# Performance work log

Measured on AMD Instinct MI355X. Metric: run time of the kernel, lower is better.

Reference implementation:

```python
import jax, jax.numpy as jnp
import numpy as np

# Dims: lifted grid is N_X x N_Y, input signal has N_IN dims (= N_X*N_Y).
N_X, N_Y, N_IN = 32, 32, 1024
FILT = 33              # resolution-filter taps (odd, centered)
SIGMA0 = 0.1           # resolution_filter_initial_sigma (step 0 of decay schedule)
EPS = 1e-7


def _resolution_filter(sigma):
    # Gaussian taps on normalized coords in ~[-1, 1], normalized to sum 1.
    t = (jnp.arange(FILT, dtype=jnp.float32) - FILT // 2) * (2.0 / FILT)
    k = jnp.exp(-0.5 * jnp.square(t / sigma))
    return k / jnp.sum(k)


def _interpolate_lifting_map(lm_raw, filt):
    # Circular 1-D convolution of the generator parametrization with the
    # Gaussian resolution filter along the input-signal axis.
    P = N_X * N_Y
    pad = FILT // 2
    v = lm_raw.reshape(P, 1, N_IN)
    v = jnp.concatenate([v[..., -pad:], v, v[..., :pad]], axis=-1)  # wrap pad
    k = filt.reshape(1, 1, FILT)
    out = jax.lax.conv_general_dilated(
        v, k, window_strides=(1,), padding='VALID',
        dimension_numbers=('NCH', 'OIH', 'NCH'))
    return out.reshape(N_X, N_Y, N_IN)


def setup_inputs() -> dict:
    key = jax.random.key(0)
    k1, k2 = jax.random.split(key)
    x = jax.random.normal(k1, (16384, N_IN), dtype=jnp.float32)
    lm_raw = jax.random.normal(k2, (N_X, N_Y, N_IN), dtype=jnp.float32) / np.float32(np.sqrt(N_IN))
    return {"x": x, "lm_raw": lm_raw}


def reference(x, lm_raw):
    # _demean_and_normalize_input: per-sample demean + std-normalize.
    mu = jnp.mean(x, axis=-1, keepdims=True)
    sd = jnp.std(x, axis=-1, keepdims=True)
    xn = (x - mu) / (sd + EPS)
    # _sample_resolution_filter + _interpolate_lifting_map
    filt = _resolution_filter(jnp.asarray(SIGMA0, dtype=jnp.float32))
    lm = _interpolate_lifting_map(lm_raw, filt)  # [n_x, n_y, n_in]
    # _lift: y[b, i, j] = sum_n lm[i, j, n] * x[b, n]
    y = jnp.einsum('xyn,bn->bxy', lm, xn)
    return y
```

## Files before the change

### kernel.cpp

```cpp
#include <hip/hip_runtime.h>
#include <hip/hip_bf16.h>

#define N_IN   1024
#define N_P    1024
#define FILT   33
#define PAD    16

typedef __attribute__((ext_vector_type(8))) __bf16 bf16x8;
typedef __attribute__((ext_vector_type(4))) float  f32x4;

#define GLB(p) ((const __attribute__((address_space(1))) unsigned int*)(p))
#define LDSP(p) ((__attribute__((address_space(3))) unsigned int*)(p))

__device__ __forceinline__ unsigned short f2bf(float f) {
    union { __hip_bfloat16 h; unsigned short u; } cv;
    cv.h = __float2bfloat16(f);
    return cv.u;
}

__global__ __launch_bounds__(256)
void normalize_kernel(const float* __restrict__ x, __hip_bfloat16* __restrict__ xn)
{
    const int lane = threadIdx.x & 63;
    const int row  = blockIdx.x * 4 + (threadIdx.x >> 6);

    const float4* xr = reinterpret_cast<const float4*>(x + (size_t)row * N_IN);
    float4 v[4];
    float s = 0.f, s2 = 0.f;
#pragma unroll
    for (int i = 0; i < 4; i++) {
        v[i] = xr[i * 64 + lane];
        s  += v[i].x + v[i].y + v[i].z + v[i].w;
        s2 += v[i].x * v[i].x + v[i].y * v[i].y + v[i].z * v[i].z + v[i].w * v[i].w;
    }
#pragma unroll
    for (int off = 32; off > 0; off >>= 1) {
        s  += __shfl_xor(s,  off, 64);
        s2 += __shfl_xor(s2, off, 64);
    }
    const float mu  = s * (1.0f / N_IN);
    const float var = fmaxf(s2 * (1.0f / N_IN) - mu * mu, 0.0f);
    const float inv = 1.0f / (sqrtf(var) + 1e-7f);

    ushort4* outv = reinterpret_cast<ushort4*>(xn + (size_t)row * N_IN);
#pragma unroll
    for (int i = 0; i < 4; i++) {
        ushort4 o;
        o.x = f2bf((v[i].x - mu) * inv);
        o.y = f2bf((v[i].y - mu) * inv);
        o.z = f2bf((v[i].z - mu) * inv);
        o.w = f2bf((v[i].w - mu) * inv);
        outv[i * 64 + lane] = o;
    }
}

__global__ __launch_bounds__(256)
void conv_kernel(const float* __restrict__ lm_raw, __hip_bfloat16* __restrict__ lm)
{
    __shared__ float row[N_IN];
    __shared__ float fw[FILT];
    const int tid = threadIdx.x;
    const int p   = blockIdx.x;

    if (tid < FILT) {
        float t = (tid - PAD) * (2.0f / FILT);
        float u = t * 10.0f;
        fw[tid] = expf(-0.5f * u * u);
    }
    reinterpret_cast<float4*>(row)[tid] =
        reinterpret_cast<const float4*>(lm_raw + (size_t)p * N_IN)[tid];
    __syncthreads();

    float fsum = 0.f;
#pragma unroll
    for (int f = 0; f < FILT; f++) fsum += fw[f];
    const float inv = 1.0f / fsum;

    const int n0 = tid * 4;
    float o[4] = {0.f, 0.f, 0.f, 0.f};
#pragma unroll
    for (int f = 0; f < FILT; f++) {
        const float w = fw[f];
#pragma unroll
        for (int j = 0; j < 4; j++)
            o[j] += w * row[(n0 + j + f - PAD) & (N_IN - 1)];
    }
    ushort4 ov;
    ov.x = f2bf(o[0] * inv);
    ov.y = f2bf(o[1] * inv);
    ov.z = f2bf(o[2] * inv);
    ov.w = f2bf(o[3] * inv);
    reinterpret_cast<ushort4*>(lm + (size_t)p * N_IN)[tid] = ov;
}

__global__ __launch_bounds__(512, 2)
void gemm_bt2(const __hip_bfloat16* __restrict__ A,
              const __hip_bfloat16* __restrict__ B,
              float* __restrict__ C,
              int M, int N, int K)
{
    constexpr int BK = 32;
    __shared__ char smem[4][32768];

    const int tid = threadIdx.x;
    const int l   = tid & 63;
    const int w   = tid >> 6;
    const int wr  = w >> 2;
    const int wc  = w & 3;

    const int o    = blockIdx.x;
    const int lin  = (o & 7) * (gridDim.x >> 3) + (o >> 3);
    const int tn   = lin & 3;
    const int tm   = lin >> 2;
    const size_t bm = (size_t)tm * 256;
    const size_t bn = (size_t)tn * 256;

    const int srow = w * 16 + (l >> 2);
    const int scol = 16 * ((l & 3) ^ ((l >> 3) & 3));
    const char* gA = (const char*)(A + (bm + srow) * (size_t)K) + scol;
    const char* gB = (const char*)(B + (bn + srow) * (size_t)K) + scol;
    const size_t rowstep = (size_t)128 * K * 2;

#define STAGE(t, b) do {                                                        \
    const char* a0_ = gA + (size_t)(t) * (BK * 2);                              \
    const char* b0_ = gB + (size_t)(t) * (BK * 2);                              \
    char* La_ = &smem[(b)][0]     + w * 1024;                                   \
    char* Lb_ = &smem[(b)][16384] + w * 1024;                                   \
    __builtin_amdgcn_global_load_lds(GLB(a0_),           LDSP(La_),        16, 0, 0); \
    __builtin_amdgcn_global_load_lds(GLB(a0_ + rowstep), LDSP(La_ + 8192), 16, 0, 0); \
    __builtin_amdgcn_global_load_lds(GLB(b0_),           LDSP(Lb_),        16, 0, 0); \
    __builtin_amdgcn_global_load_lds(GLB(b0_ + rowstep), LDSP(Lb_ + 8192), 16, 0, 0); \
} while (0)

    const int lr = l & 15;
    const int kb = l >> 4;
    const int rslot = 16 * (kb ^ ((lr >> 1) & 3));

    f32x4 acc[8][4] = {};

    const int NT = K / BK;

    STAGE(0, 0);
    STAGE(1, 1);
    STAGE(2, 2);

    for (int t = 0; t < NT; ++t) {
        asm volatile("s_waitcnt lgkmcnt(0)" ::: "memory");
        if (t < NT - 2)       asm volatile("s_waitcnt vmcnt(8)" ::: "memory");
        else if (t == NT - 2) asm volatile("s_waitcnt vmcnt(4)" ::: "memory");
        else                  asm volatile("s_waitcnt vmcnt(0)" ::: "memory");
        __builtin_amdgcn_s_barrier();
        asm volatile("" ::: "memory");

        if (t + 3 < NT) STAGE(t + 3, (t + 3) & 3);

        const char* Ab = &smem[t & 3][0];
        const char* Bb = &smem[t & 3][16384];

        bf16x8 bfr[4], afr[8];
#pragma unroll
        for (int n = 0; n < 4; n++)
            bfr[n] = *(const bf16x8*)(Bb + (wc * 64 + n * 16 + lr) * 64 + rslot);
#pragma unroll
        for (int m = 0; m < 8; m++)
            afr[m] = *(const bf16x8*)(Ab + (wr * 128 + m * 16 + lr) * 64 + rslot);

#pragma unroll
        for (int m = 0; m < 8; m++)
#pragma unroll
            for (int n = 0; n < 4; n++)
                acc[m][n] = __builtin_amdgcn_mfma_f32_16x16x32_bf16(afr[m], bfr[n], acc[m][n], 0, 0, 0);
    }
#undef STAGE

    const int crow = (l >> 4) * 4;
    const int ccol = l & 15;
#pragma unroll
    for (int m = 0; m < 8; m++)
#pragma unroll
        for (int n = 0; n < 4; n++) {
#pragma unroll
            for (int r = 0; r < 4; r++) {
                const size_t row = bm + wr * 128 + m * 16 + crow + r;
                const size_t col = bn + wc * 64 + n * 16 + ccol;
                C[row * N + col] = acc[m][n][r];
            }
        }
}

extern "C" void kernel_launch(void* const* d_in, const int* in_sizes, int n_in,
                              void* d_out, int out_size, void* d_ws, size_t ws_size,
                              hipStream_t stream) {
    const float* x      = (const float*)d_in[0];
    const float* lm_raw = (const float*)d_in[1];
    float* out = (float*)d_out;

    const int M = in_sizes[0] / N_IN;

    __hip_bfloat16* xn = (__hip_bfloat16*)d_ws;
    __hip_bfloat16* lm = (__hip_bfloat16*)((char*)d_ws + (size_t)M * N_IN * 2);

    normalize_kernel<<<M / 4, 256, 0, stream>>>(x, xn);
    conv_kernel<<<N_P, 256, 0, stream>>>(lm_raw, lm);

    const int nblk = (M / 256) * (N_P / 256);
    gemm_bt2<<<nblk, dim3(512), 0, stream>>>(xn, lm, out, M, N_P, N_IN);
}
```

Before: 65.58 us.

## Shrink GEMM tile to 256x128 with 3-stage LDS ring and higher occupancy

Changes the GEMM block tile from 256x256 to 256x128, rearranges the 8 waves as a 4x2 grid with 64x64 sub-tiles each, and cuts the LDS ring from 4 to 3 stages (prefetch distance 2). Launch bounds are raised to 4 blocks per CU and MFMA issue is wrapped in s_setprio. The aim is to double the block count and raise occupancy so latency is hidden by concurrent blocks, at the cost of more B-tile reloads per output element and a shallower prefetch pipeline.

New measurement: 65.77 us. About the same (+0.3%).

```diff
diff --git a/kernel.cpp b/kernel.cpp
--- a/kernel.cpp
+++ b/kernel.cpp
@@ -93,27 +93,27 @@
     reinterpret_cast<ushort4*>(lm + (size_t)p * N_IN)[tid] = ov;
 }
 
-__global__ __launch_bounds__(512, 2)
-void gemm_bt2(const __hip_bfloat16* __restrict__ A,
+__global__ __launch_bounds__(512, 4)
+void gemm_bt3(const __hip_bfloat16* __restrict__ A,
               const __hip_bfloat16* __restrict__ B,
               float* __restrict__ C,
               int M, int N, int K)
 {
     constexpr int BK = 32;
-    __shared__ char smem[4][32768];
+    __shared__ char smem[3][24576];
 
     const int tid = threadIdx.x;
     const int l   = tid & 63;
     const int w   = tid >> 6;
-    const int wr  = w >> 2;
-    const int wc  = w & 3;
+    const int wm  = w >> 1;
+    const int wn  = w & 1;
 
     const int o    = blockIdx.x;
     const int lin  = (o & 7) * (gridDim.x >> 3) + (o >> 3);
-    const int tn   = lin & 3;
-    const int tm   = lin >> 2;
+    const int tn   = lin & 7;
+    const int tm   = lin >> 3;
     const size_t bm = (size_t)tm * 256;
-    const size_t bn = (size_t)tn * 256;
+    const size_t bn = (size_t)tn * 128;
 
     const int srow = w * 16 + (l >> 2);
     const int scol = 16 * ((l & 3) ^ ((l >> 3) & 3));
@@ -129,60 +129,66 @@
     __builtin_amdgcn_global_load_lds(GLB(a0_),           LDSP(La_),        16, 0, 0); \
     __builtin_amdgcn_global_load_lds(GLB(a0_ + rowstep), LDSP(La_ + 8192), 16, 0, 0); \
     __builtin_amdgcn_global_load_lds(GLB(b0_),           LDSP(Lb_),        16, 0, 0); \
-    __builtin_amdgcn_global_load_lds(GLB(b0_ + rowstep), LDSP(Lb_ + 8192), 16, 0, 0); \
 } while (0)
 
     const int lr = l & 15;
     const int kb = l >> 4;
     const int rslot = 16 * (kb ^ ((lr >> 1) & 3));
-
-    f32x4 acc[8][4] = {};
+    const int abase = (wm * 64 + lr) * 64 + rslot;
+    const int bbase = 16384 + (wn * 64 + lr) * 64 + rslot;
+
+    f32x4 acc[4][4] = {};
 
     const int NT = K / BK;
 
     STAGE(0, 0);
     STAGE(1, 1);
-    STAGE(2, 2);
-
+
+    int buf = 0;
     for (int t = 0; t < NT; ++t) {
         asm volatile("s_waitcnt lgkmcnt(0)" ::: "memory");
-        if (t < NT - 2)       asm volatile("s_waitcnt vmcnt(8)" ::: "memory");
-        else if (t == NT - 2) asm volatile("s_waitcnt vmcnt(4)" ::: "memory");
-        else                  asm volatile("s_waitcnt vmcnt(0)" ::: "memory");
+        if (t < NT - 1) asm volatile("s_waitcnt vmcnt(3)" ::: "memory");
+        else            asm volatile("s_waitcnt vmcnt(0)" ::: "memory");
         __builtin_amdgcn_s_barrier();
         asm volatile("" ::: "memory");
 
-        if (t + 3 < NT) STAGE(t + 3, (t + 3) & 3);
-
-        const char* Ab = &smem[t & 3][0];
-        const char* Bb = &smem[t & 3][16384];
-
-        bf16x8 bfr[4], afr[8];
-#pragma unroll
-        for (int n = 0; n < 4; n++)
-            bfr[n] = *(const bf16x8*)(Bb + (wc * 64 + n * 16 + lr) * 64 + rslot);
-#pragma unroll
-        for (int m = 0; m < 8; m++)
-            afr[m] = *(const bf16x8*)(Ab + (wr * 128 + m * 16 + lr) * 64 + rslot);
-
-#pragma unroll
-        for (int m = 0; m < 8; m++)
+        {
+            const int t2 = t + 2;
+            if (t2 < NT) {
+                int b2 = buf + 2; if (b2 >= 3) b2 -= 3;
+                STAGE(t2, b2);
+            }
+        }
+
+        const char* Sb = &smem[buf][0];
+        bf16x8 afr[4], bfr[4];
+#pragma unroll
+        for (int n = 0; n < 4; n++) bfr[n] = *(const bf16x8*)(Sb + bbase + n * 1024);
+#pragma unroll
+        for (int m = 0; m < 4; m++) afr[m] = *(const bf16x8*)(Sb + abase + m * 1024);
+
+        __builtin_amdgcn_s_setprio(1);
+#pragma unroll
+        for (int m = 0; m < 4; m++)
 #pragma unroll
             for (int n = 0; n < 4; n++)
                 acc[m][n] = __builtin_amdgcn_mfma_f32_16x16x32_bf16(afr[m], bfr[n], acc[m][n], 0, 0, 0);
+        __builtin_amdgcn_s_setprio(0);
+
+        if (++buf == 3) buf = 0;
     }
 #undef STAGE
 
     const int crow = (l >> 4) * 4;
     const int ccol = l & 15;
 #pragma unroll
-    for (int m = 0; m < 8; m++)
+    for (int m = 0; m < 4; m++)
 #pragma unroll
         for (int n = 0; n < 4; n++) {
 #pragma unroll
             for (int r = 0; r < 4; r++) {
-                const size_t row = bm + wr * 128 + m * 16 + crow + r;
-                const size_t col = bn + wc * 64 + n * 16 + ccol;
+                const size_t row = bm + wm * 64 + m * 16 + crow + r;
+                const size_t col = bn + wn * 64 + n * 16 + ccol;
                 C[row * N + col] = acc[m][n][r];
             }
         }
@@ -203,6 +209,6 @@
     normalize_kernel<<<M / 4, 256, 0, stream>>>(x, xn);
     conv_kernel<<<N_P, 256, 0, stream>>>(lm_raw, lm);
 
-    const int nblk = (M / 256) * (N_P / 256);
-    gemm_bt2<<<nblk, dim3(512), 0, stream>>>(xn, lm, out, M, N_P, N_IN);
-}
+    const int nblk = (M / 256) * (N_P / 128);
+    gemm_bt3<<<nblk, dim3(512), 0, stream>>>(xn, lm, out, M, N_P, N_IN);
+}
```

## Make GEMM waves load their own LDS tiles and raise MFMA priority

Applied to the files above, without the earlier changes.

The GEMM staging changes so that each wave issues global-to-LDS loads only for the A rows and B rows it later reads. This removes the need for a block-wide lgkmcnt drain before the barrier. Prefetch depth drops from three tiles ahead to two, and each wave now waits only on its own vmcnt. The MFMA block is wrapped in s_setprio to favour compute issue. The cost is redundant loading: waves sharing rows or columns load and write the same data, which roughly triples per-block global-to-LDS traffic.

Result: slower. 75.61 us (+15.3%).

```diff
diff --git a/kernel.cpp b/kernel.cpp
--- a/kernel.cpp
+++ b/kernel.cpp
@@ -94,19 +94,18 @@
 }
 
 __global__ __launch_bounds__(512, 2)
-void gemm_bt2(const __hip_bfloat16* __restrict__ A,
-              const __hip_bfloat16* __restrict__ B,
-              float* __restrict__ C,
-              int M, int N, int K)
+void gemm_async(const __hip_bfloat16* __restrict__ A,
+                const __hip_bfloat16* __restrict__ B,
+                float* __restrict__ C,
+                int M, int N, int K)
 {
-    constexpr int BK = 32;
     __shared__ char smem[4][32768];
 
     const int tid = threadIdx.x;
     const int l   = tid & 63;
     const int w   = tid >> 6;
-    const int wr  = w >> 2;
-    const int wc  = w & 3;
+    const int wm  = w >> 2;
+    const int wn  = w & 3;
 
     const int o    = blockIdx.x;
     const int lin  = (o & 7) * (gridDim.x >> 3) + (o >> 3);
@@ -115,63 +114,67 @@
     const size_t bm = (size_t)tm * 256;
     const size_t bn = (size_t)tn * 256;
 
-    const int srow = w * 16 + (l >> 2);
+    const int sgrp = l >> 2;
     const int scol = 16 * ((l & 3) ^ ((l >> 3) & 3));
-    const char* gA = (const char*)(A + (bm + srow) * (size_t)K) + scol;
-    const char* gB = (const char*)(B + (bn + srow) * (size_t)K) + scol;
-    const size_t rowstep = (size_t)128 * K * 2;
-
-#define STAGE(t, b) do {                                                        \
-    const char* a0_ = gA + (size_t)(t) * (BK * 2);                              \
-    const char* b0_ = gB + (size_t)(t) * (BK * 2);                              \
-    char* La_ = &smem[(b)][0]     + w * 1024;                                   \
-    char* Lb_ = &smem[(b)][16384] + w * 1024;                                   \
-    __builtin_amdgcn_global_load_lds(GLB(a0_),           LDSP(La_),        16, 0, 0); \
-    __builtin_amdgcn_global_load_lds(GLB(a0_ + rowstep), LDSP(La_ + 8192), 16, 0, 0); \
-    __builtin_amdgcn_global_load_lds(GLB(b0_),           LDSP(Lb_),        16, 0, 0); \
-    __builtin_amdgcn_global_load_lds(GLB(b0_ + rowstep), LDSP(Lb_ + 8192), 16, 0, 0); \
+    const char* gAw = (const char*)(A + (bm + wm * 128 + sgrp) * (size_t)K) + scol;
+    const char* gBw = (const char*)(B + (bn + wn * 64  + sgrp) * (size_t)K) + scol;
+    const size_t chunkstep = (size_t)16 * K * 2;
+
+#define STAGE_W(t, b) do {                                                      \
+    const char* a_ = gAw + (size_t)(t) * 64;                                    \
+    const char* b_ = gBw + (size_t)(t) * 64;                                    \
+    char* L_ = &smem[(b)][0];                                                   \
+    _Pragma("unroll")                                                           \
+    for (int c_ = 0; c_ < 8; c_++)                                              \
+        __builtin_amdgcn_global_load_lds(GLB(a_ + c_ * chunkstep),              \
+            LDSP(L_ + wm * 8192 + c_ * 1024), 16, 0, 0);                        \
+    _Pragma("unroll")                                                           \
+    for (int c_ = 0; c_ < 4; c_++)                                              \
+        __builtin_amdgcn_global_load_lds(GLB(b_ + c_ * chunkstep),              \
+            LDSP(L_ + 16384 + wn * 4096 + c_ * 1024), 16, 0, 0);                \
 } while (0)
 
     const int lr = l & 15;
     const int kb = l >> 4;
     const int rslot = 16 * (kb ^ ((lr >> 1) & 3));
+    const int abase = (wm * 128 + lr) * 64 + rslot;
+    const int bbase = 16384 + (wn * 64 + lr) * 64 + rslot;
 
     f32x4 acc[8][4] = {};
-
-    const int NT = K / BK;
-
-    STAGE(0, 0);
-    STAGE(1, 1);
-    STAGE(2, 2);
+    const int NT = K / 32;
+
+    STAGE_W(0, 0);
+    STAGE_W(1, 1);
 
     for (int t = 0; t < NT; ++t) {
-        asm volatile("s_waitcnt lgkmcnt(0)" ::: "memory");
-        if (t < NT - 2)       asm volatile("s_waitcnt vmcnt(8)" ::: "memory");
-        else if (t == NT - 2) asm volatile("s_waitcnt vmcnt(4)" ::: "memory");
-        else                  asm volatile("s_waitcnt vmcnt(0)" ::: "memory");
         __builtin_amdgcn_s_barrier();
         asm volatile("" ::: "memory");
 
-        if (t + 3 < NT) STAGE(t + 3, (t + 3) & 3);
-
-        const char* Ab = &smem[t & 3][0];
-        const char* Bb = &smem[t & 3][16384];
-
-        bf16x8 bfr[4], afr[8];
-#pragma unroll
-        for (int n = 0; n < 4; n++)
-            bfr[n] = *(const bf16x8*)(Bb + (wc * 64 + n * 16 + lr) * 64 + rslot);
-#pragma unroll
-        for (int m = 0; m < 8; m++)
-            afr[m] = *(const bf16x8*)(Ab + (wr * 128 + m * 16 + lr) * 64 + rslot);
-
+        if (t + 2 < NT) {
+            STAGE_W(t + 2, (t + 2) & 3);
+            asm volatile("s_waitcnt vmcnt(24)" ::: "memory");
+        } else if (t == NT - 2) {
+            asm volatile("s_waitcnt vmcnt(12)" ::: "memory");
+        } else {
+            asm volatile("s_waitcnt vmcnt(0)" ::: "memory");
+        }
+
+        const char* S = &smem[t & 3][0];
+        bf16x8 afr[8], bfr[4];
+#pragma unroll
+        for (int n = 0; n < 4; n++) bfr[n] = *(const bf16x8*)(S + bbase + n * 1024);
+#pragma unroll
+        for (int m = 0; m < 8; m++) afr[m] = *(const bf16x8*)(S + abase + m * 1024);
+
+        __builtin_amdgcn_s_setprio(1);
 #pragma unroll
         for (int m = 0; m < 8; m++)
 #pragma unroll
             for (int n = 0; n < 4; n++)
                 acc[m][n] = __builtin_amdgcn_mfma_f32_16x16x32_bf16(afr[m], bfr[n], acc[m][n], 0, 0, 0);
-    }
-#undef STAGE
+        __builtin_amdgcn_s_setprio(0);
+    }
+#undef STAGE_W
 
     const int crow = (l >> 4) * 4;
     const int ccol = l & 15;
@@ -181,8 +184,8 @@
         for (int n = 0; n < 4; n++) {
 #pragma unroll
             for (int r = 0; r < 4; r++) {
-                const size_t row = bm + wr * 128 + m * 16 + crow + r;
-                const size_t col = bn + wc * 64 + n * 16 + ccol;
+                const size_t row = bm + wm * 128 + m * 16 + crow + r;
+                const size_t col = bn + wn * 64 + n * 16 + ccol;
                 C[row * N + col] = acc[m][n][r];
             }
         }
@@ -204,5 +207,5 @@
     conv_kernel<<<N_P, 256, 0, stream>>>(lm_raw, lm);
 
     const int nblk = (M / 256) * (N_P / 256);
-    gemm_bt2<<<nblk, dim3(512), 0, stream>>>(xn, lm, out, M, N_P, N_IN);
-}
+    gemm_async<<<nblk, dim3(512), 0, stream>>>(xn, lm, out, M, N_P, N_IN);
+}
```
